# Optimization experiments

Hardware: AMD Instinct MI355X
Metric: run time of the kernel (lower is better)

The kernel has to match this reference:

```python
import jax, jax.numpy as jnp
import numpy as np

B, S, H, NH = 2, 2048, 4096, 32
D = H // NH  # head_dim = 128


def setup_inputs() -> dict:
    key = jax.random.key(0)
    ks = jax.random.split(key, 9)
    s = 1.0 / np.sqrt(H)
    return {
        "hidden_state": jax.random.normal(ks[0], (B, S, H), jnp.float32),
        "Wq": jax.random.normal(ks[1], (H, H), jnp.float32) * s,
        "bq": jax.random.normal(ks[2], (H,), jnp.float32) * 0.01,
        "Wk": jax.random.normal(ks[3], (D, H), jnp.float32) * s,
        "bk": jax.random.normal(ks[4], (D,), jnp.float32) * 0.01,
        "Wv": jax.random.normal(ks[5], (D, H), jnp.float32) * s,
        "bv": jax.random.normal(ks[6], (D,), jnp.float32) * 0.01,
        "Wo": jax.random.normal(ks[7], (H, H), jnp.float32) * s,
        "bo": jax.random.normal(ks[8], (H,), jnp.float32) * 0.01,
    }


def reference(hidden_state, Wq, bq, Wk, bk, Wv, bv, Wo, bo):
    b = hidden_state.shape[0]
    # Projections (torch Linear: x @ W.T + b)
    q = hidden_state @ Wq.T + bq              # (b, s, H)
    k = hidden_state @ Wk.T + bk              # (b, s, D) single shared KV head
    v = hidden_state @ Wv.T + bv              # (b, s, D)
    q = q.reshape(b, -1, NH, D).transpose(0, 2, 1, 3)  # (b, nh, s, d)
    # scores: broadcast the single K head across all query heads
    scale = 1.0 / jnp.sqrt(jnp.float32(D))
    scores = jnp.einsum("bhqd,bkd->bhqk", q, k) * scale   # (b, nh, s, s)
    probs = jax.nn.softmax(scores, axis=-1)
    out = jnp.einsum("bhqk,bkd->bhqd", probs, v)           # (b, nh, s, d)
    # Faithful to source: transpose(-1,-2) then view(b, -1, nh*d)
    out = jnp.swapaxes(out, -1, -2).reshape(b, -1, NH * D)  # (b, s, H) scrambled layout
    return out @ Wo.T + bo
```

## Files before the change

### kernel.cpp

```cpp
#include <hip/hip_runtime.h>
#include <hip/hip_bf16.h>

typedef __attribute__((ext_vector_type(8))) short bf16x8;
typedef __attribute__((ext_vector_type(4))) float f32x4;

__device__ __forceinline__ unsigned short f2bf(float f) {
    unsigned u = __builtin_bit_cast(unsigned, f);
    u += 0x7FFFu + ((u >> 16) & 1u);
    return (unsigned short)(u >> 16);
}

__device__ __forceinline__ void async16(const void* g, void* l) {
    __builtin_amdgcn_global_load_lds(
        (const __attribute__((address_space(1))) unsigned int*)g,
        (__attribute__((address_space(3))) unsigned int*)l, 16, 0, 0);
}

template <int N> __device__ __forceinline__ void waitv() {
    if constexpr (N == 8)      asm volatile("s_waitcnt vmcnt(8)" ::: "memory");
    else if constexpr (N == 6) asm volatile("s_waitcnt vmcnt(6)" ::: "memory");
    else if constexpr (N == 4) asm volatile("s_waitcnt vmcnt(4)" ::: "memory");
    else if constexpr (N == 3) asm volatile("s_waitcnt vmcnt(3)" ::: "memory");
    else                       asm volatile("s_waitcnt vmcnt(0)" ::: "memory");
}
#define BARF() do { __builtin_amdgcn_s_barrier(); asm volatile("" ::: "memory"); } while (0)

__global__ void cvt_f32_bf16(const float* __restrict__ x, unsigned short* __restrict__ y, int n4) {
    const int stride = gridDim.x * blockDim.x;
    for (int i = blockIdx.x * blockDim.x + threadIdx.x; i < n4; i += stride) {
        const float4 v = ((const float4*)x)[i];
        ushort4 o;
        o.x = f2bf(v.x); o.y = f2bf(v.y); o.z = f2bf(v.z); o.w = f2bf(v.w);
        ((ushort4*)y)[i] = o;
    }
}

template <int MREP, int MODE>
__global__ __launch_bounds__(512, 2) void gemm256(
    const unsigned short* __restrict__ A, const unsigned short* __restrict__ Bt,
    const float* __restrict__ b0, const float* __restrict__ b1, const float* __restrict__ b2,
    void* __restrict__ o0, unsigned short* __restrict__ o1, unsigned short* __restrict__ o2)
{
    constexpr int K = 4096, NT = 128;
    constexpr int ACALLS = MREP / 4;
    constexpr int CALLS  = ACALLS + 2;
    constexpr int ASH    = MREP * 1024;
    constexpr int SLOT   = ASH + 8192;
    __shared__ __align__(16) unsigned short lds[4 * SLOT];

    const int tid  = threadIdx.x;
    const int w    = tid >> 6, lane = tid & 63;
    const int l16  = lane & 15, quad = lane >> 4;
    const int wm   = w >> 2, wn = w & 3;

    int bx, by;
    {
        const int wg = (int)blockIdx.x;
        if constexpr (MODE == 1) {
            const int wgp = (wg & 7) * 68 + (wg >> 3);
            bx = wgp / 32; by = wgp % 32;
        } else {
            const int wgp = (wg & 7) * 32 + (wg >> 3);
            bx = wgp / 16; by = wgp % 16;
        }
    }
    const int m0 = by * (MREP * 32);
    const int n0 = bx * 256;

    const int srow = lane >> 2;
    const int schk = ((lane & 3) ^ ((lane >> 3) & 3)) * 8;
    const unsigned short* gAs[ACALLS];
#pragma unroll
    for (int c = 0; c < ACALLS; ++c)
        gAs[c] = A + (size_t)(m0 + (w * ACALLS + c) * 16 + srow) * K + schk;
    const unsigned short* gBs[2];
#pragma unroll
    for (int c = 0; c < 2; ++c)
        gBs[c] = Bt + (size_t)(n0 + (w * 2 + c) * 16 + srow) * K + schk;

    const int swz8 = (quad ^ ((l16 >> 1) & 3)) * 8;
    const int aoff = (wm * (MREP * 16) + l16) * 32 + swz8;
    const int boff = ASH + (wn * 64 + l16) * 32 + swz8;

    f32x4 acc[MREP][4] = {};

#define STAGE(tt) do { \
    unsigned short* lb = &lds[((tt) & 3) * SLOT]; \
    _Pragma("unroll") \
    for (int c = 0; c < ACALLS; ++c) \
        async16(gAs[c] + (tt) * 32, lb + (w * ACALLS + c) * 512); \
    _Pragma("unroll") \
    for (int c = 0; c < 2; ++c) \
        async16(gBs[c] + (tt) * 32, lb + ASH + (w * 2 + c) * 512); \
} while (0)

#define BODY(tt) do { \
    const unsigned short* lb = &lds[((tt) & 3) * SLOT]; \
    bf16x8 af[MREP], bfr[4]; \
    _Pragma("unroll") \
    for (int i = 0; i < MREP; ++i) af[i] = *(const bf16x8*)(lb + aoff + i * 512); \
    _Pragma("unroll") \
    for (int j = 0; j < 4; ++j)    bfr[j] = *(const bf16x8*)(lb + boff + j * 512); \
    __builtin_amdgcn_s_setprio(1); \
    _Pragma("unroll") \
    for (int i = 0; i < MREP; ++i) { \
        _Pragma("unroll") \
        for (int j = 0; j < 4; ++j) \
            acc[i][j] = __builtin_amdgcn_mfma_f32_16x16x32_bf16(af[i], bfr[j], acc[i][j], 0, 0, 0); \
    } \
    __builtin_amdgcn_s_setprio(0); \
} while (0)

    STAGE(0); STAGE(1); STAGE(2);
    for (int t = 0; t < NT - 3; ++t) {
        waitv<CALLS * 2>();
        BARF();
        STAGE(t + 3);
        BODY(t);
    }
    waitv<CALLS * 2>(); BARF(); BODY(NT - 3);
    waitv<CALLS>();     BARF(); BODY(NT - 2);
    waitv<0>();         BARF(); BODY(NT - 1);

#undef STAGE
#undef BODY

    if constexpr (MODE == 0) {
        float* C = (float*)o0;
#pragma unroll
        for (int j = 0; j < 4; ++j) {
            const int n = n0 + wn * 64 + j * 16 + l16;
            const float bb = b0[n];
#pragma unroll
            for (int i = 0; i < MREP; ++i) {
                const int mb = m0 + wm * (MREP * 16) + i * 16 + quad * 4;
#pragma unroll
                for (int r = 0; r < 4; ++r)
                    C[(size_t)(mb + r) * 4096 + n] = acc[i][j][r] + bb;
            }
        }
    } else {
        unsigned short* q_out = (unsigned short*)o0;
        const int nw0 = n0 + wn * 64;
        if (nw0 < 4096) {
#pragma unroll
            for (int j = 0; j < 4; ++j) {
                const int n = nw0 + j * 16 + l16;
                const float bb = b0[n];
#pragma unroll
                for (int i = 0; i < MREP; ++i) {
                    const int mb = m0 + wm * (MREP * 16) + i * 16 + quad * 4;
#pragma unroll
                    for (int r = 0; r < 4; ++r)
                        q_out[(size_t)(mb + r) * 4096 + n] = f2bf(acc[i][j][r] + bb);
                }
            }
        } else if (nw0 < 4224) {
#pragma unroll
            for (int j = 0; j < 4; ++j) {
                const int d = nw0 - 4096 + j * 16 + l16;
                const float bb = b1[d];
#pragma unroll
                for (int i = 0; i < MREP; ++i) {
                    const int mb = m0 + wm * (MREP * 16) + i * 16 + quad * 4;
#pragma unroll
                    for (int r = 0; r < 4; ++r)
                        o1[(size_t)(mb + r) * 128 + d] = f2bf(acc[i][j][r] + bb);
                }
            }
        } else {
#pragma unroll
            for (int j = 0; j < 4; ++j) {
                const int d = nw0 - 4224 + j * 16 + l16;
                const float bb = b2[d];
#pragma unroll
                for (int i = 0; i < MREP; ++i) {
                    const int mb = m0 + wm * (MREP * 16) + i * 16 + quad * 4;
                    ushort4 o;
                    o.x = f2bf(acc[i][j][0] + bb);
                    o.y = f2bf(acc[i][j][1] + bb);
                    o.z = f2bf(acc[i][j][2] + bb);
                    o.w = f2bf(acc[i][j][3] + bb);
                    *(ushort4*)(o2 + (size_t)((mb >> 11) * 128 + d) * 2048 + (mb & 2047)) = o;
                }
            }
        }
    }
}

__global__ __launch_bounds__(256) void attn_mqa(
    const unsigned short* __restrict__ Q,
    const unsigned short* __restrict__ Kb,
    const unsigned short* __restrict__ vT,
    unsigned short* __restrict__ scr)
{
    constexpr int S = 2048, D = 128, H = 4096;
    constexpr float CSC = 0.0883883476483184f * 1.4426950408889634f;

    __shared__ __align__(16) unsigned short lds[25600];

    const int tid = threadIdx.x;
    const int w = tid >> 6, lane = tid & 63;
    const int l16 = lane & 15, quad = lane >> 4;
    const int qb = blockIdx.x & 15;
    const int h  = (blockIdx.x >> 4) & 31;
    const int b  = blockIdx.x >> 9;
    const int q0 = qb * 128;

    bf16x8 qf[2][4];
#pragma unroll
    for (int mi = 0; mi < 2; ++mi)
#pragma unroll
        for (int ks = 0; ks < 4; ++ks)
            qf[mi][ks] = *(const bf16x8*)(Q + (size_t)(b * S + q0 + w * 32 + mi * 16 + l16) * H
                                            + h * D + ks * 32 + quad * 8);

    f32x4 Oa[2][8] = {};
    float l_run[2][4] = {};

    const unsigned short* gK = Kb + (size_t)(b * S + l16) * D + quad * 8;
    const unsigned short* gV = vT + (size_t)(b * 128 + l16) * 2048 + quad * 8;

    for (int kv0 = 0; kv0 < S; kv0 += 64) {
        __syncthreads();
#pragma unroll
        for (int t = 0; t < 4; ++t) {
            const int c = w * 4 + t;
            const int ct = c >> 2, ks = c & 3;
            async16(gK + (size_t)(kv0 + ct * 16) * D + ks * 32, &lds[c * 512]);
            const int nt = c >> 1, kk = c & 1;
            async16(gV + (size_t)(nt * 16) * 2048 + kv0 + kk * 32, &lds[8192 + c * 512]);
        }
        __syncthreads();

        f32x4 sf[2][4] = {};
#pragma unroll
        for (int ct = 0; ct < 4; ++ct)
#pragma unroll
            for (int ks = 0; ks < 4; ++ks) {
                const bf16x8 kf = *(const bf16x8*)&lds[(ct * 4 + ks) * 512 + lane * 8];
#pragma unroll
                for (int mi = 0; mi < 2; ++mi)
                    sf[mi][ct] = __builtin_amdgcn_mfma_f32_16x16x32_bf16(qf[mi][ks], kf, sf[mi][ct], 0, 0, 0);
            }

#pragma unroll
        for (int mi = 0; mi < 2; ++mi)
#pragma unroll
            for (int ct = 0; ct < 4; ++ct)
#pragma unroll
                for (int i = 0; i < 4; ++i) {
                    const float p = exp2f(sf[mi][ct][i] * CSC);
                    l_run[mi][i] += p;
                    lds[16384 + (w * 2 + mi) * 1152 + (quad * 4 + i) * 72 + ct * 16 + l16] = f2bf(p);
                }
        asm volatile("s_waitcnt lgkmcnt(0)" ::: "memory");

        bf16x8 ap[2][2];
#pragma unroll
        for (int mi = 0; mi < 2; ++mi)
#pragma unroll
            for (int kk = 0; kk < 2; ++kk)
                ap[mi][kk] = *(const bf16x8*)&lds[16384 + (w * 2 + mi) * 1152 + l16 * 72 + kk * 32 + quad * 8];
#pragma unroll
        for (int nt = 0; nt < 8; ++nt)
#pragma unroll
            for (int kk = 0; kk < 2; ++kk) {
                const bf16x8 vf = *(const bf16x8*)&lds[8192 + (nt * 2 + kk) * 512 + lane * 8];
#pragma unroll
                for (int mi = 0; mi < 2; ++mi)
                    Oa[mi][nt] = __builtin_amdgcn_mfma_f32_16x16x32_bf16(ap[mi][kk], vf, Oa[mi][nt], 0, 0, 0);
            }
    }

    float inv[2][4];
#pragma unroll
    for (int mi = 0; mi < 2; ++mi)
#pragma unroll
        for (int i = 0; i < 4; ++i) {
            float l = l_run[mi][i];
            l += __shfl_xor(l, 1);
            l += __shfl_xor(l, 2);
            l += __shfl_xor(l, 4);
            l += __shfl_xor(l, 8);
            inv[mi][i] = 1.f / l;
        }

    __syncthreads();
#pragma unroll
    for (int mi = 0; mi < 2; ++mi)
#pragma unroll
        for (int nt = 0; nt < 8; ++nt)
#pragma unroll
            for (int i = 0; i < 4; ++i)
                lds[(nt * 16 + l16) * 136 + w * 32 + mi * 16 + quad * 4 + i] =
                    f2bf(Oa[mi][nt][i] * inv[mi][i]);
    __syncthreads();

    const int d = tid >> 1, qh = tid & 1;
    unsigned short* op = scr + (size_t)(b * S + h * 64 + (d >> 1)) * H + (d & 1) * 2048 + q0 + qh * 64;
#pragma unroll
    for (int j = 0; j < 8; ++j)
        *(int4*)(op + j * 8) = *(const int4*)&lds[d * 136 + qh * 64 + j * 8];
}

extern "C" void kernel_launch(void* const* d_in, const int* in_sizes, int n_in,
                              void* d_out, int out_size, void* d_ws, size_t ws_size,
                              hipStream_t stream) {
    (void)in_sizes; (void)n_in; (void)out_size; (void)ws_size;
    const float* hidden = (const float*)d_in[0];
    const float* Wq = (const float*)d_in[1];
    const float* bq = (const float*)d_in[2];
    const float* Wk = (const float*)d_in[3];
    const float* bk = (const float*)d_in[4];
    const float* Wv = (const float*)d_in[5];
    const float* bv = (const float*)d_in[6];
    const float* Wo = (const float*)d_in[7];
    const float* bo = (const float*)d_in[8];

    char* ws = (char*)d_ws;
    const size_t MB = 1048576;
    unsigned short* hb   = (unsigned short*)(ws);
    unsigned short* scr  = hb;
    unsigned short* Wcat = (unsigned short*)(ws + 32 * MB);
    unsigned short* Wob  = Wcat;
    unsigned short* q_b  = (unsigned short*)(ws + 68 * MB);
    unsigned short* k_b  = (unsigned short*)(ws + 100 * MB);
    unsigned short* vT   = (unsigned short*)(ws + 101 * MB);

    cvt_f32_bf16<<<1024, 256, 0, stream>>>(hidden, hb, 16777216 / 4);
    cvt_f32_bf16<<<1024, 256, 0, stream>>>(Wq, Wcat, 16777216 / 4);
    cvt_f32_bf16<<<256, 256, 0, stream>>>(Wk, Wcat + 16777216, 524288 / 4);
    cvt_f32_bf16<<<256, 256, 0, stream>>>(Wv, Wcat + 17301504, 524288 / 4);

    gemm256<4, 1><<<dim3(544), 512, 0, stream>>>(hb, Wcat, bq, bk, bv,
                                                 (void*)q_b, k_b, vT);
    cvt_f32_bf16<<<1024, 256, 0, stream>>>(Wo, Wob, 16777216 / 4);
    attn_mqa<<<1024, 256, 0, stream>>>(q_b, k_b, vT, scr);
    gemm256<8, 0><<<dim3(256), 512, 0, stream>>>(scr, Wob, bo, nullptr, nullptr,
                                                 (void*)d_out, nullptr, nullptr);
}
```

Before: 780.1 us.

## Keep attention probabilities in registers via transposed QK^T and permlane swaps

Swaps the MFMA operand order for the QK^T product so each lane holds scores along the key dimension. The probabilities are then packed to bf16 with v_cvt_pk_bf16_f32 and rearranged with permlane32/permlane16 swaps to form the A operand of the PV MFMA directly. This removes the per-iteration LDS round trip for the probability tile, shrinks shared memory, and simplifies the row-sum reduction. The risk is that the permlane reshuffle does not map the fragment layout correctly, and it adds cross-lane ops to the inner loop.

After: 753.6 us. -3.4%, faster.

```diff
diff --git a/kernel.cpp b/kernel.cpp
--- a/kernel.cpp
+++ b/kernel.cpp
@@ -3,6 +3,8 @@
 
 typedef __attribute__((ext_vector_type(8))) short bf16x8;
 typedef __attribute__((ext_vector_type(4))) float f32x4;
+typedef __attribute__((ext_vector_type(4))) unsigned int u32x4;
+typedef __attribute__((ext_vector_type(2))) unsigned int u32x2;
 
 __device__ __forceinline__ unsigned short f2bf(float f) {
     unsigned u = __builtin_bit_cast(unsigned, f);
@@ -24,6 +26,15 @@
     else                       asm volatile("s_waitcnt vmcnt(0)" ::: "memory");
 }
 #define BARF() do { __builtin_amdgcn_s_barrier(); asm volatile("" ::: "memory"); } while (0)
+
+__device__ __forceinline__ void pl32(unsigned &a, unsigned &b) {
+    u32x2 r = __builtin_amdgcn_permlane32_swap(a, b, false, false);
+    a = r[0]; b = r[1];
+}
+__device__ __forceinline__ void pl16(unsigned &a, unsigned &b) {
+    u32x2 r = __builtin_amdgcn_permlane16_swap(a, b, false, false);
+    a = r[0]; b = r[1];
+}
 
 __global__ void cvt_f32_bf16(const float* __restrict__ x, unsigned short* __restrict__ y, int n4) {
     const int stride = gridDim.x * blockDim.x;
@@ -197,7 +208,7 @@
     constexpr int S = 2048, D = 128, H = 4096;
     constexpr float CSC = 0.0883883476483184f * 1.4426950408889634f;
 
-    __shared__ __align__(16) unsigned short lds[25600];
+    __shared__ __align__(16) unsigned short lds[17536];
 
     const int tid = threadIdx.x;
     const int w = tid >> 6, lane = tid & 63;
@@ -216,7 +227,7 @@
                                             + h * D + ks * 32 + quad * 8);
 
     f32x4 Oa[2][8] = {};
-    float l_run[2][4] = {};
+    float l_run[2] = {};
 
     const unsigned short* gK = Kb + (size_t)(b * S + l16) * D + quad * 8;
     const unsigned short* gV = vT + (size_t)(b * 128 + l16) * 2048 + quad * 8;
@@ -241,27 +252,34 @@
                 const bf16x8 kf = *(const bf16x8*)&lds[(ct * 4 + ks) * 512 + lane * 8];
 #pragma unroll
                 for (int mi = 0; mi < 2; ++mi)
-                    sf[mi][ct] = __builtin_amdgcn_mfma_f32_16x16x32_bf16(qf[mi][ks], kf, sf[mi][ct], 0, 0, 0);
-            }
-
-#pragma unroll
-        for (int mi = 0; mi < 2; ++mi)
-#pragma unroll
-            for (int ct = 0; ct < 4; ++ct)
-#pragma unroll
-                for (int i = 0; i < 4; ++i) {
-                    const float p = exp2f(sf[mi][ct][i] * CSC);
-                    l_run[mi][i] += p;
-                    lds[16384 + (w * 2 + mi) * 1152 + (quad * 4 + i) * 72 + ct * 16 + l16] = f2bf(p);
-                }
-        asm volatile("s_waitcnt lgkmcnt(0)" ::: "memory");
-
-        bf16x8 ap[2][2];
-#pragma unroll
-        for (int mi = 0; mi < 2; ++mi)
-#pragma unroll
-            for (int kk = 0; kk < 2; ++kk)
-                ap[mi][kk] = *(const bf16x8*)&lds[16384 + (w * 2 + mi) * 1152 + l16 * 72 + kk * 32 + quad * 8];
+                    sf[mi][ct] = __builtin_amdgcn_mfma_f32_16x16x32_bf16(kf, qf[mi][ks], sf[mi][ct], 0, 0, 0);
+            }
+
+        bf16x8 pa[2][2];
+#pragma unroll
+        for (int mi = 0; mi < 2; ++mi) {
+            unsigned cw[4][2];
+#pragma unroll
+            for (int ct = 0; ct < 4; ++ct) {
+                const float p0 = exp2f(sf[mi][ct][0] * CSC);
+                const float p1 = exp2f(sf[mi][ct][1] * CSC);
+                const float p2 = exp2f(sf[mi][ct][2] * CSC);
+                const float p3 = exp2f(sf[mi][ct][3] * CSC);
+                l_run[mi] += (p0 + p1) + (p2 + p3);
+                asm("v_cvt_pk_bf16_f32 %0, %1, %2" : "=v"(cw[ct][0]) : "v"(p0), "v"(p1));
+                asm("v_cvt_pk_bf16_f32 %0, %1, %2" : "=v"(cw[ct][1]) : "v"(p2), "v"(p3));
+            }
+#pragma unroll
+            for (int kk = 0; kk < 2; ++kk) {
+                unsigned c0 = cw[2 * kk][0], c1 = cw[2 * kk][1];
+                unsigned d0 = cw[2 * kk + 1][0], d1 = cw[2 * kk + 1][1];
+                pl32(c0, d0); pl16(c0, d0);
+                pl32(c1, d1); pl16(c1, d1);
+                u32x4 t4; t4[0] = c0; t4[1] = c1; t4[2] = d0; t4[3] = d1;
+                pa[mi][kk] = __builtin_bit_cast(bf16x8, t4);
+            }
+        }
+
 #pragma unroll
         for (int nt = 0; nt < 8; ++nt)
 #pragma unroll
@@ -269,22 +287,21 @@
                 const bf16x8 vf = *(const bf16x8*)&lds[8192 + (nt * 2 + kk) * 512 + lane * 8];
 #pragma unroll
                 for (int mi = 0; mi < 2; ++mi)
-                    Oa[mi][nt] = __builtin_amdgcn_mfma_f32_16x16x32_bf16(ap[mi][kk], vf, Oa[mi][nt], 0, 0, 0);
-            }
-    }
-
-    float inv[2][4];
-#pragma unroll
-    for (int mi = 0; mi < 2; ++mi)
-#pragma unroll
-        for (int i = 0; i < 4; ++i) {
-            float l = l_run[mi][i];
-            l += __shfl_xor(l, 1);
-            l += __shfl_xor(l, 2);
-            l += __shfl_xor(l, 4);
-            l += __shfl_xor(l, 8);
-            inv[mi][i] = 1.f / l;
-        }
+                    Oa[mi][nt] = __builtin_amdgcn_mfma_f32_16x16x32_bf16(pa[mi][kk], vf, Oa[mi][nt], 0, 0, 0);
+            }
+    }
+
+    float iv[2][4];
+#pragma unroll
+    for (int mi = 0; mi < 2; ++mi) {
+        float l = l_run[mi];
+        l += __shfl_xor(l, 16);
+        l += __shfl_xor(l, 32);
+        const float linv = 1.f / l;
+#pragma unroll
+        for (int i = 0; i < 4; ++i)
+            iv[mi][i] = __shfl(linv, quad * 4 + i);
+    }
 
     __syncthreads();
 #pragma unroll
@@ -294,7 +311,7 @@
 #pragma unroll
             for (int i = 0; i < 4; ++i)
                 lds[(nt * 16 + l16) * 136 + w * 32 + mi * 16 + quad * 4 + i] =
-                    f2bf(Oa[mi][nt][i] * inv[mi][i]);
+                    f2bf(Oa[mi][nt][i] * iv[mi][i]);
     __syncthreads();
 
     const int d = tid >> 1, qh = tid & 1;
```
